# Kernel tuning notes

Hardware: AMD Instinct MI355X
Metric: run time of the kernel (lower is better)

Reference implementation:

```python
import jax, jax.numpy as jnp
import numpy as np

B, N, C, H, KS = 4, 1024, 768, 12, 7
DFF = 4 * C
HD = C // H
EPS = 1e-5


def layernorm(x, g, b):
    mu = jnp.mean(x, axis=-1, keepdims=True)
    var = jnp.mean(jnp.square(x - mu), axis=-1, keepdims=True)
    return (x - mu) * jax.lax.rsqrt(var + EPS) * g + b


def setup_inputs() -> dict:
    key = jax.random.key(0)
    ks = jax.random.split(key, 16)
    s = 0.02
    return {
        "x": jax.random.normal(ks[0], (B, N, C), jnp.float32),
        "w_qkv": jax.random.normal(ks[1], (3 * C, C), jnp.float32) * s,
        "b_qkv": jnp.zeros((3 * C,), jnp.float32),
        "w_proj": jax.random.normal(ks[2], (C, C), jnp.float32) * s,
        "b_proj": jnp.zeros((C,), jnp.float32),
        "w_fc1": jax.random.normal(ks[3], (DFF, C), jnp.float32) * s,
        "b_fc1": jnp.zeros((DFF,), jnp.float32),
        "w_fc2": jax.random.normal(ks[4], (C, DFF), jnp.float32) * s,
        "b_fc2": jnp.zeros((C,), jnp.float32),
        "t_before": jnp.eye(H, dtype=jnp.float32) + s * jax.random.normal(ks[5], (H, H), jnp.float32),
        "t_after": jnp.eye(H, dtype=jnp.float32) + s * jax.random.normal(ks[6], (H, H), jnp.float32),
        "g1": jnp.ones((C,), jnp.float32), "be1": jnp.zeros((C,), jnp.float32),
        "g2": jnp.ones((C,), jnp.float32), "be2": jnp.zeros((C,), jnp.float32),
        "dw_w": jax.random.normal(ks[7], (C, 1, KS), jnp.float32) * s,
        "dw_b": jnp.zeros((C,), jnp.float32),
        "gm": jnp.ones((C,), jnp.float32), "bm": jnp.zeros((C,), jnp.float32),
    }


def reference(x, w_qkv, b_qkv, w_proj, b_proj, w_fc1, b_fc1, w_fc2, b_fc2,
              t_before, t_after, g1, be1, g2, be2, dw_w, dw_b, gm, bm):
    residual = x
    h = layernorm(x, g1, be1)
    qkv = h @ w_qkv.T + b_qkv                       # [B,N,3C]
    qkv = qkv.reshape(B, N, 3, H, HD).transpose(2, 0, 3, 1, 4)  # [3,B,H,N,HD]
    q, k, v = qkv[0], qkv[1], qkv[2]
    scale = HD ** -0.5
    attn = jnp.einsum('bhnd,bhmd->bhnm', q, k) * scale          # [B,H,N,N]
    # head mixing before softmax: attn_perm @ T_before.T over head dim
    attn = jnp.einsum('bhnm,gh->bgnm', attn, t_before)
    attn = jax.nn.softmax(attn, axis=-1)
    # head mixing after softmax
    attn = jnp.einsum('bhnm,gh->bgnm', attn, t_after)
    out = jnp.einsum('bhnm,bhmd->bhnd', attn, v)                 # [B,H,N,HD]
    out = out.transpose(0, 2, 1, 3).reshape(B, N, C)
    out = out @ w_proj.T + b_proj
    x = residual + out
    residual = x
    h = layernorm(x, g2, be2)
    # MLP transform: depthwise conv1d over tokens + layernorm
    ht = h.transpose(0, 2, 1)                                    # [B,C,N]
    ht = jax.lax.conv_general_dilated(
        ht, dw_w, window_strides=(1,), padding=[(KS // 2, KS // 2)],
        feature_group_count=C, dimension_numbers=('NCH', 'OIH', 'NCH'))
    ht = ht + dw_b[None, :, None]
    h = layernorm(ht.transpose(0, 2, 1), gm, bm)
    # standard MLP (fc1 -> GELU -> fc2)
    h = jax.nn.gelu(h @ w_fc1.T + b_fc1, approximate=False)
    h = h @ w_fc2.T + b_fc2
    return residual + h
```

## Files before the change

kernel.cpp:

```cpp
#include <hip/hip_runtime.h>


typedef unsigned short u16;
typedef __bf16 bf16x8 __attribute__((ext_vector_type(8)));
typedef u16 u16x8 __attribute__((ext_vector_type(8)));
typedef float f32x4 __attribute__((ext_vector_type(4)));

using gvoid = __attribute__((address_space(1))) const void;
using lvoid = __attribute__((address_space(3))) void;
#define GLD16(GP, LP) __builtin_amdgcn_global_load_lds((gvoid*)(GP), (lvoid*)(LP), 16, 0, 0)

__device__ __forceinline__ u16 f2b(float f) {
  unsigned u = __float_as_uint(f);
  u = (u + 0x7FFFu + ((u >> 16) & 1u)) >> 16;
  return (u16)u;
}
__device__ __forceinline__ float b2f(u16 b) { return __uint_as_float(((unsigned)b) << 16); }
__device__ __forceinline__ float gelu_exact(float x) {
  return 0.5f * x * (1.f + erff(x * 0.70710678118654752f));
}

__global__ __launch_bounds__(256) void cast_all(const float* __restrict__ s0,
                                                const float* __restrict__ s1,
                                                const float* __restrict__ s2,
                                                const float* __restrict__ s3,
                                                u16* __restrict__ d0, u16* __restrict__ d1,
                                                u16* __restrict__ d2, u16* __restrict__ d3) {
  const int n0 = 1769472 / 4, n1 = 589824 / 4, n2 = 2359296 / 4;
  int j = blockIdx.x * 256 + threadIdx.x;
  const float* src;
  u16* dst;
  if (j < n0) { src = s0; dst = d0; }
  else if ((j -= n0) < n1) { src = s1; dst = d1; }
  else if ((j -= n1) < n2) { src = s2; dst = d2; }
  else { j -= n2; src = s3; dst = d3; }
  const float4 v = ((const float4*)src)[j];
  ushort4 o;
  o.x = f2b(v.x); o.y = f2b(v.y); o.z = f2b(v.z); o.w = f2b(v.w);
  ((ushort4*)dst)[j] = o;
}

template <typename OutT>
__global__ __launch_bounds__(256) void ln_row(const float* __restrict__ x,
                                              const float* __restrict__ g,
                                              const float* __restrict__ be,
                                              OutT* __restrict__ out) {
  const long row = blockIdx.x;
  const float* xr = x + row * 768;
  OutT* yr = out + row * 768;
  const int tid = threadIdx.x;
  const int w = tid >> 6, lane = tid & 63;
  float v[3], s = 0.f, s2 = 0.f;
#pragma unroll
  for (int i = 0; i < 3; ++i) {
    v[i] = xr[tid + i * 256];
    s += v[i];
    s2 += v[i] * v[i];
  }
#pragma unroll
  for (int off = 32; off; off >>= 1) {
    s += __shfl_xor(s, off);
    s2 += __shfl_xor(s2, off);
  }
  __shared__ float red[8];
  if (lane == 0) { red[w] = s; red[w + 4] = s2; }
  __syncthreads();
  s = red[0] + red[1] + red[2] + red[3];
  s2 = red[4] + red[5] + red[6] + red[7];
  const float mu = s * (1.f / 768.f);
  const float var = s2 * (1.f / 768.f) - mu * mu;
  const float rstd = rsqrtf(var + 1e-5f);
#pragma unroll
  for (int i = 0; i < 3; ++i) {
    const int c = tid + i * 256;
    float y = (v[i] - mu) * rstd * g[c] + be[c];
    if constexpr (sizeof(OutT) == 2) yr[c] = f2b(y);
    else yr[c] = y;
  }
}

template <int TM, int TN, int ACT, bool HAS_RES, typename OutT>
__global__ __launch_bounds__(256) void gemm_bt(
    const u16* __restrict__ A, const u16* __restrict__ B, OutT* __restrict__ C,
    const float* __restrict__ bias, const float* __restrict__ res,
    int K, int lda, int ldb, int ldc, int ldr) {
  constexpr int WM = TM / 2, WN = TN / 2, MR = WM / 16, NR = WN / 16;
  __shared__ __align__(16) u16 As[2][TM * 32];
  __shared__ __align__(16) u16 Bs[2][TN * 32];
  const int tid = threadIdx.x;
  const int w = tid >> 6, lane = tid & 63;
  const int wr = w >> 1, wc = w & 1;
  const int l16 = lane & 15, lh = lane >> 4;
  const long rowA = (long)blockIdx.y * TM;
  const long colB = (long)blockIdx.x * TN;
  const int srow = tid >> 2;
  const int scol = (((tid & 3) ^ (srow & 3))) * 8;

  f32x4 acc[MR][NR];
#pragma unroll
  for (int m = 0; m < MR; ++m)
#pragma unroll
    for (int n = 0; n < NR; ++n) acc[m][n] = f32x4{0.f, 0.f, 0.f, 0.f};

  auto stage = [&](int buf, int k0) {
#pragma unroll
    for (int r = 0; r < TM / 64; ++r)
      GLD16(A + (rowA + r * 64 + srow) * (long)lda + k0 + scol, (char*)As[buf] + r * 4096 + w * 1024);
#pragma unroll
    for (int r = 0; r < TN / 64; ++r)
      GLD16(B + (colB + r * 64 + srow) * (long)ldb + k0 + scol, (char*)Bs[buf] + r * 4096 + w * 1024);
  };

  stage(0, 0);
  __syncthreads();
  const int nk = K >> 5;
  const int rx = (lh ^ (l16 & 3)) * 8;
  for (int t = 0; t < nk; ++t) {
    const int buf = t & 1;
    if (t + 1 < nk) stage(buf ^ 1, (t + 1) << 5);
    bf16x8 a[MR], bb[NR];
#pragma unroll
    for (int m = 0; m < MR; ++m)
      a[m] = *(const bf16x8*)&As[buf][(wr * WM + m * 16 + l16) * 32 + rx];
#pragma unroll
    for (int n = 0; n < NR; ++n)
      bb[n] = *(const bf16x8*)&Bs[buf][(wc * WN + n * 16 + l16) * 32 + rx];
#pragma unroll
    for (int m = 0; m < MR; ++m)
#pragma unroll
      for (int n = 0; n < NR; ++n)
        acc[m][n] = __builtin_amdgcn_mfma_f32_16x16x32_bf16(a[m], bb[n], acc[m][n], 0, 0, 0);
    __syncthreads();
  }

  const long row0 = rowA + wr * WM;
  const long col0 = colB + wc * WN;
#pragma unroll
  for (int m = 0; m < MR; ++m)
#pragma unroll
    for (int n = 0; n < NR; ++n)
#pragma unroll
      for (int r = 0; r < 4; ++r) {
        const long row = row0 + m * 16 + lh * 4 + r;
        const long col = col0 + n * 16 + l16;
        float v = acc[m][n][r];
        if (bias) v += bias[col];
        if (ACT == 1) v = gelu_exact(v);
        if (HAS_RES) v += res[row * (long)ldr + col];
        if constexpr (sizeof(OutT) == 2) C[row * (long)ldc + col] = f2b(v);
        else C[row * (long)ldc + col] = v;
      }
}

__global__ __launch_bounds__(256) void scores_mix(const u16* __restrict__ qkv,
                                                  const float* __restrict__ Tb,
                                                  u16* __restrict__ attn) {
  __shared__ __align__(16) u16 Qs[32 * 768];
  __shared__ __align__(16) u16 Ks[32 * 768];
  __shared__ float Ts[144];
  const int tid = threadIdx.x;
  const int w = tid >> 6, lane = tid & 63;
  const int b = blockIdx.z;
  const int n0 = blockIdx.y * 32, m0 = blockIdx.x * 32;
  if (tid < 144) Ts[tid] = Tb[tid];
  const char* qb = (const char*)qkv;
#pragma unroll
  for (int i = 0; i < 12; ++i) {
    const int idx = i * 256 + tid;
    const int r = idx / 96, t = idx % 96;
    const int s = t ^ (r & 7);
    const long rQ = ((long)b * 1024 + n0 + r) * 4608;
    const long rK = ((long)b * 1024 + m0 + r) * 4608;
    GLD16(qb + rQ + s * 16, (char*)Qs + (i * 256 + w * 64) * 16);
    GLD16(qb + rK + 1536 + s * 16, (char*)Ks + (i * 256 + w * 64) * 16);
  }
  __syncthreads();
  const int wr = w >> 1, wc = w & 1;
  const int l16 = lane & 15, lh = lane >> 4;
  const int x7 = l16 & 7;
  const char* Qrow = (const char*)Qs + (wr * 16 + l16) * 1536;
  const char* Krow = (const char*)Ks + (wc * 16 + l16) * 1536;
  f32x4 acc[12];
#pragma unroll
  for (int h = 0; h < 12; ++h) acc[h] = f32x4{0.f, 0.f, 0.f, 0.f};
#pragma unroll
  for (int h = 0; h < 12; ++h)
#pragma unroll
    for (int kk = 0; kk < 2; ++kk) {
      const int slot = h * 8 + kk * 4 + lh;
      const bf16x8 a = *(const bf16x8*)(Qrow + (slot ^ x7) * 16);
      const bf16x8 bb = *(const bf16x8*)(Krow + (slot ^ x7) * 16);
      acc[h] = __builtin_amdgcn_mfma_f32_16x16x32_bf16(a, bb, acc[h], 0, 0, 0);
    }
#pragma unroll
  for (int g = 0; g < 12; ++g) {
    f32x4 o = f32x4{0.f, 0.f, 0.f, 0.f};
#pragma unroll
    for (int h = 0; h < 12; ++h) o += Ts[g * 12 + h] * acc[h];
    u16* dst = attn + (((long)(b * 12 + g)) << 20) +
               (long)(n0 + wr * 16 + lh * 4) * 1024 + (m0 + wc * 16 + l16);
#pragma unroll
    for (int r = 0; r < 4; ++r) dst[r * 1024] = f2b(o[r] * 0.125f);
  }
}

__global__ __launch_bounds__(256) void softmax_mix(u16* __restrict__ attn,
                                                   const float* __restrict__ Tg) {
  const int bi = blockIdx.x >> 10;
  const int n = blockIdx.x & 1023;
  __shared__ float Ta[144];
  __shared__ float red[8];
  const int tid = threadIdx.x;
  const int w = tid >> 6, lane = tid & 63;
  if (tid < 144) Ta[tid] = Tg[tid];
  const long base = (((long)bi * 12) << 20) + (long)n * 1024;
  float p[12][4];
#pragma unroll
  for (int h = 0; h < 12; ++h) {
    const uint2 d = ((const uint2*)(attn + base + ((long)h << 20)))[tid];
    float v[4] = {b2f((u16)(d.x & 0xffff)), b2f((u16)(d.x >> 16)),
                  b2f((u16)(d.y & 0xffff)), b2f((u16)(d.y >> 16))};
    float mx = fmaxf(fmaxf(v[0], v[1]), fmaxf(v[2], v[3]));
#pragma unroll
    for (int off = 32; off; off >>= 1) mx = fmaxf(mx, __shfl_xor(mx, off));
    __syncthreads();
    if (lane == 0) red[w] = mx;
    __syncthreads();
    mx = fmaxf(fmaxf(red[0], red[1]), fmaxf(red[2], red[3]));
    float s = 0.f;
#pragma unroll
    for (int i = 0; i < 4; ++i) {
      v[i] = __expf(v[i] - mx);
      s += v[i];
    }
#pragma unroll
    for (int off = 32; off; off >>= 1) s += __shfl_xor(s, off);
    if (lane == 0) red[w + 4] = s;
    __syncthreads();
    s = red[4] + red[5] + red[6] + red[7];
    const float inv = 1.f / s;
#pragma unroll
    for (int i = 0; i < 4; ++i) p[h][i] = v[i] * inv;
  }
#pragma unroll
  for (int g = 0; g < 12; ++g) {
    float o[4] = {0.f, 0.f, 0.f, 0.f};
#pragma unroll
    for (int h = 0; h < 12; ++h) {
      const float t = Ta[g * 12 + h];
#pragma unroll
      for (int i = 0; i < 4; ++i) o[i] += t * p[h][i];
    }
    uint2 d;
    d.x = (unsigned)f2b(o[0]) | ((unsigned)f2b(o[1]) << 16);
    d.y = (unsigned)f2b(o[2]) | ((unsigned)f2b(o[3]) << 16);
    ((uint2*)(attn + base + ((long)g << 20)))[tid] = d;
  }
}

__global__ __launch_bounds__(256) void av_gemm(const u16* __restrict__ attn,
                                               const u16* __restrict__ qkv,
                                               u16* __restrict__ out) {
  __shared__ __align__(16) u16 As[2][64 * 32];
  __shared__ __align__(16) u16 Vt[2][64 * 40];
  const int tid = threadIdx.x;
  const int w = tid >> 6, lane = tid & 63;
  const int z = blockIdx.y, b = z / 12, h = z % 12;
  const u16* A = attn + ((long)z << 20);
  const u16* V = qkv + (long)b * 1024 * 2304 + 1536 + h * 64;
  const int rowA = blockIdx.x * 64;
  const int srow = tid >> 2;
  const int scol = (((tid & 3) ^ (srow & 3))) * 8;
  const int l16 = lane & 15, lh = lane >> 4;

  f32x4 acc[4];
#pragma unroll
  for (int n = 0; n < 4; ++n) acc[n] = f32x4{0.f, 0.f, 0.f, 0.f};

  auto stageA = [&](int buf, int k0) {
    GLD16(A + (long)(rowA + srow) * 1024 + k0 + scol, (char*)As[buf] + w * 1024);
  };
  auto stageV = [&](int buf, int k0) {
    u16x8 tmp;
#pragma unroll
    for (int j = 0; j < 8; ++j) tmp[j] = V[(long)(k0 + w * 8 + j) * 2304 + lane];
    *(u16x8*)&Vt[buf][lane * 40 + w * 8] = tmp;
  };

  stageA(0, 0);
  stageV(0, 0);
  __syncthreads();
  for (int t = 0; t < 32; ++t) {
    const int buf = t & 1;
    if (t < 31) { stageA(buf ^ 1, (t + 1) * 32); stageV(buf ^ 1, (t + 1) * 32); }
    const bf16x8 a = *(const bf16x8*)&As[buf][(w * 16 + l16) * 32 + (lh ^ (l16 & 3)) * 8];
    bf16x8 bv[4];
#pragma unroll
    for (int n = 0; n < 4; ++n)
      bv[n] = *(const bf16x8*)&Vt[buf][(n * 16 + l16) * 40 + lh * 8];
#pragma unroll
    for (int n = 0; n < 4; ++n)
      acc[n] = __builtin_amdgcn_mfma_f32_16x16x32_bf16(a, bv[n], acc[n], 0, 0, 0);
    __syncthreads();
  }
  const int row0 = rowA + w * 16 + lh * 4;
#pragma unroll
  for (int n = 0; n < 4; ++n)
#pragma unroll
    for (int r = 0; r < 4; ++r)
      out[((long)b * 1024 + row0 + r) * 768 + h * 64 + n * 16 + l16] = f2b(acc[n][r]);
}

__global__ __launch_bounds__(256) void dwconv4(const float* __restrict__ h2,
                                               const float* __restrict__ wgt,
                                               const float* __restrict__ bias,
                                               float* __restrict__ ct) {
  const int idx = blockIdx.x * 256 + threadIdx.x;
  const int c4 = idx % 192;
  const int n = (idx / 192) % 1024;
  const int b = idx / (192 * 1024);
  const int c = c4 * 4;
  float4 acc = ((const float4*)bias)[c4];
#pragma unroll
  for (int t = 0; t < 7; ++t) {
    const int nn = n + t - 3;
    if (nn >= 0 && nn < 1024) {
      const float4 v = *(const float4*)&h2[((long)(b << 10) + nn) * 768 + c];
      acc.x += v.x * wgt[(c + 0) * 7 + t];
      acc.y += v.y * wgt[(c + 1) * 7 + t];
      acc.z += v.z * wgt[(c + 2) * 7 + t];
      acc.w += v.w * wgt[(c + 3) * 7 + t];
    }
  }
  ((float4*)ct)[idx] = acc;
}

extern "C" void kernel_launch(void* const* d_in, const int* in_sizes, int n_in,
                              void* d_out, int out_size, void* d_ws, size_t ws_size,
                              hipStream_t stream) {
  const float* x      = (const float*)d_in[0];
  const float* w_qkv  = (const float*)d_in[1];
  const float* b_qkv  = (const float*)d_in[2];
  const float* w_proj = (const float*)d_in[3];
  const float* b_proj = (const float*)d_in[4];
  const float* w_fc1  = (const float*)d_in[5];
  const float* b_fc1  = (const float*)d_in[6];
  const float* w_fc2  = (const float*)d_in[7];
  const float* b_fc2  = (const float*)d_in[8];
  const float* t_bef  = (const float*)d_in[9];
  const float* t_aft  = (const float*)d_in[10];
  const float* g1     = (const float*)d_in[11];
  const float* be1    = (const float*)d_in[12];
  const float* g2     = (const float*)d_in[13];
  const float* be2    = (const float*)d_in[14];
  const float* dw_w   = (const float*)d_in[15];
  const float* dw_b   = (const float*)d_in[16];
  const float* gm     = (const float*)d_in[17];
  const float* bm     = (const float*)d_in[18];
  float* out = (float*)d_out;

  char* wsp = (char*)d_ws;
  size_t off = 0;
  auto alloc = [&](size_t bytes) {
    char* r = wsp + off;
    off += (bytes + 255) & ~(size_t)255;
    return r;
  };
  u16* wqkv_b  = (u16*)alloc((size_t)2304 * 768 * 2);
  u16* wproj_b = (u16*)alloc((size_t)768 * 768 * 2);
  u16* wfc1_b  = (u16*)alloc((size_t)3072 * 768 * 2);
  u16* wfc2_b  = (u16*)alloc((size_t)768 * 3072 * 2);
  u16* h1      = (u16*)alloc((size_t)4096 * 768 * 2);
  u16* attn_out = h1;
  u16* qkvb    = (u16*)alloc((size_t)4096 * 2304 * 2);
  char* attn_region = alloc((size_t)48 * 1024 * 1024 * 2);
  u16* attn = (u16*)attn_region;
  size_t ro = 0;
  auto ralloc = [&](size_t bytes) {
    char* r = attn_region + ro;
    ro += (bytes + 255) & ~(size_t)255;
    return r;
  };
  float* x2   = (float*)ralloc((size_t)4096 * 768 * 4);
  float* h2   = (float*)ralloc((size_t)4096 * 768 * 4);
  float* ct   = (float*)ralloc((size_t)4096 * 768 * 4);
  u16*   hm   = (u16*)ralloc((size_t)4096 * 768 * 2);
  u16*   fc1o = (u16*)ralloc((size_t)4096 * 3072 * 2);
  (void)ws_size; (void)n_in; (void)in_sizes; (void)out_size;

  cast_all<<<6912, 256, 0, stream>>>(w_qkv, w_proj, w_fc1, w_fc2,
                                     wqkv_b, wproj_b, wfc1_b, wfc2_b);
  ln_row<u16><<<4096, 256, 0, stream>>>(x, g1, be1, h1);
  gemm_bt<128, 64, 0, false, u16><<<dim3(36, 32), 256, 0, stream>>>(
      h1, wqkv_b, qkvb, b_qkv, nullptr, 768, 768, 768, 2304, 0);
  scores_mix<<<dim3(32, 32, 4), 256, 0, stream>>>(qkvb, t_bef, attn);
  softmax_mix<<<4096, 256, 0, stream>>>(attn, t_aft);
  av_gemm<<<dim3(16, 48), 256, 0, stream>>>(attn, qkvb, attn_out);
  gemm_bt<64, 64, 0, true, float><<<dim3(12, 64), 256, 0, stream>>>(
      attn_out, wproj_b, x2, b_proj, x, 768, 768, 768, 768, 768);
  ln_row<float><<<4096, 256, 0, stream>>>(x2, g2, be2, h2);
  dwconv4<<<3072, 256, 0, stream>>>(h2, dw_w, dw_b, ct);
  ln_row<u16><<<4096, 256, 0, stream>>>(ct, gm, bm, hm);
  gemm_bt<128, 64, 1, false, u16><<<dim3(48, 32), 256, 0, stream>>>(
      hm, wfc1_b, fc1o, b_fc1, nullptr, 768, 768, 768, 3072, 0);
  gemm_bt<64, 64, 0, true, float><<<dim3(12, 64), 256, 0, stream>>>(
      fc1o, wfc2_b, out, b_fc2, x2, 3072, 3072, 3072, 768, 768);
}
```

Before: 474.3 us.

## Swap MFMA operands for row-contiguous vectorized epilogue stores; load scores Q/K directly

The MFMA operand order is swapped in the GEMM, scores and AV kernels. Each lane now holds four consecutive columns of one row, so epilogues can use float4 and packed-bf16 uint2 loads and stores instead of scattered scalar ones. The scores_mix kernel drops its large LDS staging of Q and K and reads fragments straight from global memory. Each warp now computes two 16x16 key tiles sharing one Q fragment, so the grid is halved. This removes LDS occupancy pressure but relies on cache hits for the repeated global fragment reads.

```diff
diff --git a/kernel.cpp b/kernel.cpp
--- a/kernel.cpp
+++ b/kernel.cpp
@@ -18,6 +18,9 @@
 __device__ __forceinline__ float b2f(u16 b) { return __uint_as_float(((unsigned)b) << 16); }
 __device__ __forceinline__ float gelu_exact(float x) {
   return 0.5f * x * (1.f + erff(x * 0.70710678118654752f));
+}
+__device__ __forceinline__ unsigned pk2(float a, float b) {
+  return (unsigned)f2b(a) | ((unsigned)f2b(b) << 16);
 }
 
 __global__ __launch_bounds__(256) void cast_all(const float* __restrict__ s0,
@@ -96,11 +99,11 @@
   const int srow = tid >> 2;
   const int scol = (((tid & 3) ^ (srow & 3))) * 8;
 
-  f32x4 acc[MR][NR];
-#pragma unroll
-  for (int m = 0; m < MR; ++m)
-#pragma unroll
-    for (int n = 0; n < NR; ++n) acc[m][n] = f32x4{0.f, 0.f, 0.f, 0.f};
+  f32x4 acc[NR][MR];
+#pragma unroll
+  for (int n = 0; n < NR; ++n)
+#pragma unroll
+    for (int m = 0; m < MR; ++m) acc[n][m] = f32x4{0.f, 0.f, 0.f, 0.f};
 
   auto stage = [&](int buf, int k0) {
 #pragma unroll
@@ -126,81 +129,100 @@
     for (int n = 0; n < NR; ++n)
       bb[n] = *(const bf16x8*)&Bs[buf][(wc * WN + n * 16 + l16) * 32 + rx];
 #pragma unroll
-    for (int m = 0; m < MR; ++m)
-#pragma unroll
-      for (int n = 0; n < NR; ++n)
-        acc[m][n] = __builtin_amdgcn_mfma_f32_16x16x32_bf16(a[m], bb[n], acc[m][n], 0, 0, 0);
+    for (int n = 0; n < NR; ++n)
+#pragma unroll
+      for (int m = 0; m < MR; ++m)
+        acc[n][m] = __builtin_amdgcn_mfma_f32_16x16x32_bf16(bb[n], a[m], acc[n][m], 0, 0, 0);
     __syncthreads();
   }
 
   const long row0 = rowA + wr * WM;
   const long col0 = colB + wc * WN;
 #pragma unroll
-  for (int m = 0; m < MR; ++m)
-#pragma unroll
-    for (int n = 0; n < NR; ++n)
-#pragma unroll
-      for (int r = 0; r < 4; ++r) {
-        const long row = row0 + m * 16 + lh * 4 + r;
-        const long col = col0 + n * 16 + l16;
-        float v = acc[m][n][r];
-        if (bias) v += bias[col];
-        if (ACT == 1) v = gelu_exact(v);
-        if (HAS_RES) v += res[row * (long)ldr + col];
-        if constexpr (sizeof(OutT) == 2) C[row * (long)ldc + col] = f2b(v);
-        else C[row * (long)ldc + col] = v;
+  for (int m = 0; m < MR; ++m) {
+    const long row = row0 + m * 16 + l16;
+#pragma unroll
+    for (int n = 0; n < NR; ++n) {
+      const long colb = col0 + n * 16 + lh * 4;
+      f32x4 v = acc[n][m];
+      if (bias) {
+        const float4 bv = *(const float4*)&bias[colb];
+        v[0] += bv.x; v[1] += bv.y; v[2] += bv.z; v[3] += bv.w;
       }
+      if (ACT == 1) {
+#pragma unroll
+        for (int r = 0; r < 4; ++r) v[r] = gelu_exact(v[r]);
+      }
+      if (HAS_RES) {
+        const float4 rv = *(const float4*)&res[row * (long)ldr + colb];
+        v[0] += rv.x; v[1] += rv.y; v[2] += rv.z; v[3] += rv.w;
+      }
+      if constexpr (sizeof(OutT) == 2) {
+        uint2 d;
+        d.x = pk2(v[0], v[1]);
+        d.y = pk2(v[2], v[3]);
+        *(uint2*)&C[row * (long)ldc + colb] = d;
+      } else {
+        float4 d = {v[0], v[1], v[2], v[3]};
+        *(float4*)&C[row * (long)ldc + colb] = d;
+      }
+    }
+  }
 }
 
 __global__ __launch_bounds__(256) void scores_mix(const u16* __restrict__ qkv,
                                                   const float* __restrict__ Tb,
                                                   u16* __restrict__ attn) {
-  __shared__ __align__(16) u16 Qs[32 * 768];
-  __shared__ __align__(16) u16 Ks[32 * 768];
   __shared__ float Ts[144];
   const int tid = threadIdx.x;
+  if (tid < 144) Ts[tid] = Tb[tid];
+  __syncthreads();
   const int w = tid >> 6, lane = tid & 63;
+  const int l16 = lane & 15, lh = lane >> 4;
   const int b = blockIdx.z;
-  const int n0 = blockIdx.y * 32, m0 = blockIdx.x * 32;
-  if (tid < 144) Ts[tid] = Tb[tid];
+  const int m0 = blockIdx.x * 64 + (w & 1) * 32;
+  const int n0 = blockIdx.y * 32 + (w >> 1) * 16;
   const char* qb = (const char*)qkv;
-#pragma unroll
-  for (int i = 0; i < 12; ++i) {
-    const int idx = i * 256 + tid;
-    const int r = idx / 96, t = idx % 96;
-    const int s = t ^ (r & 7);
-    const long rQ = ((long)b * 1024 + n0 + r) * 4608;
-    const long rK = ((long)b * 1024 + m0 + r) * 4608;
-    GLD16(qb + rQ + s * 16, (char*)Qs + (i * 256 + w * 64) * 16);
-    GLD16(qb + rK + 1536 + s * 16, (char*)Ks + (i * 256 + w * 64) * 16);
-  }
-  __syncthreads();
-  const int wr = w >> 1, wc = w & 1;
-  const int l16 = lane & 15, lh = lane >> 4;
-  const int x7 = l16 & 7;
-  const char* Qrow = (const char*)Qs + (wr * 16 + l16) * 1536;
-  const char* Krow = (const char*)Ks + (wc * 16 + l16) * 1536;
-  f32x4 acc[12];
-#pragma unroll
-  for (int h = 0; h < 12; ++h) acc[h] = f32x4{0.f, 0.f, 0.f, 0.f};
+  const long qrow = ((long)(b << 10) + n0 + l16) * 4608 + lh * 16;
+  const long krow0 = ((long)(b << 10) + m0 + l16) * 4608 + 1536 + lh * 16;
+  const long krow1 = krow0 + 16 * 4608;
+
+  f32x4 acc[12][2];
+#pragma unroll
+  for (int h = 0; h < 12; ++h) {
+    acc[h][0] = f32x4{0.f, 0.f, 0.f, 0.f};
+    acc[h][1] = f32x4{0.f, 0.f, 0.f, 0.f};
+  }
 #pragma unroll
   for (int h = 0; h < 12; ++h)
 #pragma unroll
     for (int kk = 0; kk < 2; ++kk) {
-      const int slot = h * 8 + kk * 4 + lh;
-      const bf16x8 a = *(const bf16x8*)(Qrow + (slot ^ x7) * 16);
-      const bf16x8 bb = *(const bf16x8*)(Krow + (slot ^ x7) * 16);
-      acc[h] = __builtin_amdgcn_mfma_f32_16x16x32_bf16(a, bb, acc[h], 0, 0, 0);
-    }
+      const int off = h * 128 + kk * 64;
+      const bf16x8 q  = *(const bf16x8*)(qb + qrow + off);
+      const bf16x8 k0 = *(const bf16x8*)(qb + krow0 + off);
+      const bf16x8 k1 = *(const bf16x8*)(qb + krow1 + off);
+      acc[h][0] = __builtin_amdgcn_mfma_f32_16x16x32_bf16(k0, q, acc[h][0], 0, 0, 0);
+      acc[h][1] = __builtin_amdgcn_mfma_f32_16x16x32_bf16(k1, q, acc[h][1], 0, 0, 0);
+    }
+  u16* abase = attn + (((long)(b * 12)) << 20) + (long)(n0 + l16) * 1024 + m0 + lh * 4;
 #pragma unroll
   for (int g = 0; g < 12; ++g) {
-    f32x4 o = f32x4{0.f, 0.f, 0.f, 0.f};
-#pragma unroll
-    for (int h = 0; h < 12; ++h) o += Ts[g * 12 + h] * acc[h];
-    u16* dst = attn + (((long)(b * 12 + g)) << 20) +
-               (long)(n0 + wr * 16 + lh * 4) * 1024 + (m0 + wc * 16 + l16);
-#pragma unroll
-    for (int r = 0; r < 4; ++r) dst[r * 1024] = f2b(o[r] * 0.125f);
+    f32x4 o0 = f32x4{0.f, 0.f, 0.f, 0.f};
+    f32x4 o1 = f32x4{0.f, 0.f, 0.f, 0.f};
+#pragma unroll
+    for (int h = 0; h < 12; ++h) {
+      const float t = Ts[g * 12 + h];
+      o0 += t * acc[h][0];
+      o1 += t * acc[h][1];
+    }
+    uint2 d0, d1;
+    d0.x = pk2(o0[0] * 0.125f, o0[1] * 0.125f);
+    d0.y = pk2(o0[2] * 0.125f, o0[3] * 0.125f);
+    d1.x = pk2(o1[0] * 0.125f, o1[1] * 0.125f);
+    d1.y = pk2(o1[2] * 0.125f, o1[3] * 0.125f);
+    u16* dst = abase + ((long)g << 20);
+    *(uint2*)dst = d0;
+    *(uint2*)(dst + 16) = d1;
   }
 }
 
@@ -252,8 +274,8 @@
       for (int i = 0; i < 4; ++i) o[i] += t * p[h][i];
     }
     uint2 d;
-    d.x = (unsigned)f2b(o[0]) | ((unsigned)f2b(o[1]) << 16);
-    d.y = (unsigned)f2b(o[2]) | ((unsigned)f2b(o[3]) << 16);
+    d.x = pk2(o[0], o[1]);
+    d.y = pk2(o[2], o[3]);
     ((uint2*)(attn + base + ((long)g << 20)))[tid] = d;
   }
 }
@@ -300,15 +322,18 @@
       bv[n] = *(const bf16x8*)&Vt[buf][(n * 16 + l16) * 40 + lh * 8];
 #pragma unroll
     for (int n = 0; n < 4; ++n)
-      acc[n] = __builtin_amdgcn_mfma_f32_16x16x32_bf16(a, bv[n], acc[n], 0, 0, 0);
+      acc[n] = __builtin_amdgcn_mfma_f32_16x16x32_bf16(bv[n], a, acc[n], 0, 0, 0);
     __syncthreads();
   }
-  const int row0 = rowA + w * 16 + lh * 4;
-#pragma unroll
-  for (int n = 0; n < 4; ++n)
-#pragma unroll
-    for (int r = 0; r < 4; ++r)
-      out[((long)b * 1024 + row0 + r) * 768 + h * 64 + n * 16 + l16] = f2b(acc[n][r]);
+  const int tok = rowA + w * 16 + l16;
+  u16* obase = out + ((long)(b << 10) + tok) * 768 + h * 64 + lh * 4;
+#pragma unroll
+  for (int df = 0; df < 4; ++df) {
+    uint2 d;
+    d.x = pk2(acc[df][0], acc[df][1]);
+    d.y = pk2(acc[df][2], acc[df][3]);
+    *(uint2*)(obase + df * 16) = d;
+  }
 }
 
 __global__ __launch_bounds__(256) void dwconv4(const float* __restrict__ h2,
@@ -393,7 +418,7 @@
   ln_row<u16><<<4096, 256, 0, stream>>>(x, g1, be1, h1);
   gemm_bt<128, 64, 0, false, u16><<<dim3(36, 32), 256, 0, stream>>>(
       h1, wqkv_b, qkvb, b_qkv, nullptr, 768, 768, 768, 2304, 0);
-  scores_mix<<<dim3(32, 32, 4), 256, 0, stream>>>(qkvb, t_bef, attn);
+  scores_mix<<<dim3(16, 32, 4), 256, 0, stream>>>(qkvb, t_bef, attn);
   softmax_mix<<<4096, 256, 0, stream>>>(attn, t_aft);
   av_gemm<<<dim3(16, 48), 256, 0, stream>>>(attn, qkvb, attn_out);
   gemm_bt<64, 64, 0, true, float><<<dim3(12, 64), 256, 0, stream>>>(
```

New measurement: 485.8 us. 1.02x slower.
